# Performance work log

Measured on AMD Instinct MI355X. Metric: run time of the kernel, lower is better.

The kernel has to match this reference:

```python
import jax, jax.numpy as jnp
import numpy as np

N = 1_048_576   # flattened tokens
C = 128         # classes
IGNORE = 0
GAMMA = 1.0     # FocalLoss bug: alpha default (1) becomes self.gamma
BETA = 1.0      # ClassficationAndMDCA: self.beta = alpha = 1.0


def setup_inputs() -> dict:
    key = jax.random.key(0)
    k1, k2 = jax.random.split(key)
    inputs = jax.random.normal(k1, (N, C), dtype=jnp.float32)
    targets = jax.random.randint(k2, (N,), 0, C, dtype=jnp.int64)
    return {"inputs": inputs, "targets": targets}


def reference(inputs, targets):
    # ignore_index filtering expressed as masked reductions (jit-friendly)
    mask = (targets != IGNORE)
    maskf = mask.astype(inputs.dtype)               # [N]
    nvalid = jnp.sum(maskf)

    # Focal loss: -(1-pt)^gamma * log pt, mean over valid tokens
    logp = jax.nn.log_softmax(inputs, axis=1)       # [N, C]
    logpt = jnp.take_along_axis(logp, targets[:, None], axis=1)[:, 0]  # [N]
    pt = jnp.exp(logpt)
    focal = -((1.0 - pt) ** GAMMA) * logpt
    loss_cls = jnp.sum(focal * maskf) / nvalid

    # MDCA: per-class |mean confidence - mean label frequency|, mean over classes
    probs = jnp.exp(logp)                           # softmax, reuse log_softmax
    avg_conf = jnp.sum(probs * maskf[:, None], axis=0) / nvalid        # [C]
    avg_count = jnp.zeros((C,), inputs.dtype).at[targets].add(maskf) / nvalid  # [C]
    loss_cal = jnp.mean(jnp.abs(avg_conf - avg_count))

    return loss_cls + BETA * loss_cal
```

## Files before the change

kernel.cpp:

```cpp
#include <hip/hip_runtime.h>

#define NC 128
#define BLOCK 256
#define GRID 2048

__global__ void cmdca_init(float* __restrict__ acc) {
    int i = threadIdx.x;
    if (i < 2 * NC + 2) acc[i] = 0.0f;
}

__device__ __forceinline__ float half_sum32(float v) {
    v += __int_as_float(__builtin_amdgcn_ds_swizzle(__float_as_int(v), 0x041F));
    v += __int_as_float(__builtin_amdgcn_ds_swizzle(__float_as_int(v), 0x081F));
    v += __int_as_float(__builtin_amdgcn_ds_swizzle(__float_as_int(v), 0x101F));
    v += __int_as_float(__builtin_amdgcn_ds_swizzle(__float_as_int(v), 0x201F));
    v += __int_as_float(__builtin_amdgcn_ds_swizzle(__float_as_int(v), 0x401F));
    return v;
}

__global__ __launch_bounds__(BLOCK) void cmdca_main(const float* __restrict__ in,
                                                    const int* __restrict__ tgt,
                                                    float* __restrict__ acc,
                                                    int nrows) {
    const int lane  = threadIdx.x & 63;
    const int l31   = lane & 31;
    const int half  = lane >> 5;
    const int wave  = blockIdx.x * (BLOCK >> 6) + (threadIdx.x >> 6);
    const int nwaves = GRID * (BLOCK >> 6);

    float conf0 = 0.f, conf1 = 0.f, conf2 = 0.f, conf3 = 0.f;
    float cnt0  = 0.f, cnt1  = 0.f, cnt2  = 0.f, cnt3  = 0.f;
    float focal = 0.f, nval  = 0.f;

    auto process = [&](int pair) {
        int myrow = pair * 2 + half;
        int okrow = (myrow < nrows);
        int r = okrow ? myrow : (nrows - 1);
        const float4 x = *reinterpret_cast<const float4*>(in + (size_t)r * NC + l31 * 4);
        int t = tgt[r];
        float e0 = __expf(x.x), e1 = __expf(x.y), e2 = __expf(x.z), e3 = __expf(x.w);
        float s = half_sum32((e0 + e1) + (e2 + e3));
        float invs = 1.0f / s;
        float logZ = __logf(s);
        int te = t & 3;
        float xsel = (te == 0) ? x.x : (te == 1) ? x.y : (te == 2) ? x.z : x.w;
        int srclane = (lane & 32) + (t >> 2);
        float xt = __int_as_float(__builtin_amdgcn_ds_bpermute(srclane << 2,
                                                               __float_as_int(xsel)));
        float logpt = xt - logZ;
        float pt = __expf(logpt);
        float valid = (t != 0 && okrow) ? 1.0f : 0.0f;
        nval  += valid;
        focal += valid * (-(1.0f - pt) * logpt);
        float vs = valid * invs;
        conf0 += vs * e0; conf1 += vs * e1; conf2 += vs * e2; conf3 += vs * e3;
        float inc = (l31 == (t >> 2)) ? valid : 0.f;
        cnt0 += (te == 0) ? inc : 0.f;
        cnt1 += (te == 1) ? inc : 0.f;
        cnt2 += (te == 2) ? inc : 0.f;
        cnt3 += (te == 3) ? inc : 0.f;
    };

    const int npairs = (nrows + 1) >> 1;
    int p = wave;
    for (; p + nwaves < npairs; p += 2 * nwaves) {
        process(p);
        process(p + nwaves);
    }
    for (; p < npairs; p += nwaves) process(p);

    __shared__ float sconf[NC];
    __shared__ float scnt[NC];
    __shared__ float sfn[2];
    if (threadIdx.x < NC) { sconf[threadIdx.x] = 0.f; scnt[threadIdx.x] = 0.f; }
    if (threadIdx.x < 2)  sfn[threadIdx.x] = 0.f;
    __syncthreads();
    int cb = 4 * l31;
    atomicAdd(&sconf[cb + 0], conf0);
    atomicAdd(&sconf[cb + 1], conf1);
    atomicAdd(&sconf[cb + 2], conf2);
    atomicAdd(&sconf[cb + 3], conf3);
    atomicAdd(&scnt[cb + 0], cnt0);
    atomicAdd(&scnt[cb + 1], cnt1);
    atomicAdd(&scnt[cb + 2], cnt2);
    atomicAdd(&scnt[cb + 3], cnt3);
    if (l31 == 0) {
        atomicAdd(&sfn[0], focal);
        atomicAdd(&sfn[1], nval);
    }
    __syncthreads();
    if (threadIdx.x < NC) {
        atomicAdd(&acc[threadIdx.x],      sconf[threadIdx.x]);
        atomicAdd(&acc[NC + threadIdx.x], scnt[threadIdx.x]);
    }
    if (threadIdx.x == 0) {
        atomicAdd(&acc[2 * NC],     sfn[0]);
        atomicAdd(&acc[2 * NC + 1], sfn[1]);
    }
}

__global__ void cmdca_fin(const float* __restrict__ acc, float* __restrict__ out) {
    int c = threadIdx.x;
    float nvalid = acc[2 * NC + 1];
    float diff = fabsf(acc[c] - acc[NC + c]) / nvalid;
    #pragma unroll
    for (int o = 32; o; o >>= 1) diff += __shfl_xor(diff, o);
    __shared__ float sh[2];
    if ((threadIdx.x & 63) == 0) sh[threadIdx.x >> 6] = diff;
    __syncthreads();
    if (threadIdx.x == 0) {
        float loss_cal = (sh[0] + sh[1]) / (float)NC;
        float loss_cls = acc[2 * NC] / nvalid;
        out[0] = loss_cls + loss_cal;
    }
}

extern "C" void kernel_launch(void* const* d_in, const int* in_sizes, int n_in,
                              void* d_out, int out_size, void* d_ws, size_t ws_size,
                              hipStream_t stream) {
    const float* in  = (const float*)d_in[0];
    const int*   tgt = (const int*)d_in[1];
    float* out = (float*)d_out;
    float* acc = (float*)d_ws;
    int nrows = in_sizes[0] / NC;

    hipLaunchKernelGGL(cmdca_init, dim3(1), dim3(512), 0, stream, acc);
    hipLaunchKernelGGL(cmdca_main, dim3(GRID), dim3(BLOCK), 0, stream, in, tgt, acc, nrows);
    hipLaunchKernelGGL(cmdca_fin,  dim3(1), dim3(NC), 0, stream, acc, out);
}
```

Before: 146.6 us.

## Use DPP row reductions and readlane gathers, batch four row-pair loads before compute

Replaces the ds_swizzle half-wave sum with DPP row shifts/broadcast plus readlane of the half totals, and replaces the ds_bpermute target gather with scalar readlanes. The main loop now issues four independent row-pair loads before computing, so more memory requests are in flight per wave. Together these aim to cut LDS-path shuffle latency and expose more memory-level parallelism in a bandwidth-bound reduction, at the cost of higher register pressure from holding four float4s.

```diff
diff --git a/kernel.cpp b/kernel.cpp
--- a/kernel.cpp
+++ b/kernel.cpp
@@ -9,12 +9,18 @@
     if (i < 2 * NC + 2) acc[i] = 0.0f;
 }
 
-__device__ __forceinline__ float half_sum32(float v) {
-    v += __int_as_float(__builtin_amdgcn_ds_swizzle(__float_as_int(v), 0x041F));
-    v += __int_as_float(__builtin_amdgcn_ds_swizzle(__float_as_int(v), 0x081F));
-    v += __int_as_float(__builtin_amdgcn_ds_swizzle(__float_as_int(v), 0x101F));
-    v += __int_as_float(__builtin_amdgcn_ds_swizzle(__float_as_int(v), 0x201F));
-    v += __int_as_float(__builtin_amdgcn_ds_swizzle(__float_as_int(v), 0x401F));
+template <int CTRL>
+__device__ __forceinline__ float dpp_add(float v) {
+    int s = __builtin_amdgcn_update_dpp(0, __float_as_int(v), CTRL, 0xF, 0xF, true);
+    return v + __int_as_float(s);
+}
+
+__device__ __forceinline__ float half_sum_dpp(float v) {
+    v = dpp_add<0x111>(v);
+    v = dpp_add<0x112>(v);
+    v = dpp_add<0x114>(v);
+    v = dpp_add<0x118>(v);
+    v = dpp_add<0x142>(v);
     return v;
 }
 
@@ -32,24 +38,34 @@
     float cnt0  = 0.f, cnt1  = 0.f, cnt2  = 0.f, cnt3  = 0.f;
     float focal = 0.f, nval  = 0.f;
 
-    auto process = [&](int pair) {
+    auto load = [&](int pair, float4& x, int& t, int& ok) {
         int myrow = pair * 2 + half;
-        int okrow = (myrow < nrows);
-        int r = okrow ? myrow : (nrows - 1);
-        const float4 x = *reinterpret_cast<const float4*>(in + (size_t)r * NC + l31 * 4);
-        int t = tgt[r];
+        ok = (myrow < nrows);
+        int r = ok ? myrow : (nrows - 1);
+        x = *reinterpret_cast<const float4*>(in + (size_t)r * NC + l31 * 4);
+        t = tgt[r];
+    };
+
+    auto compute = [&](const float4& x, int t, int ok) {
         float e0 = __expf(x.x), e1 = __expf(x.y), e2 = __expf(x.z), e3 = __expf(x.w);
-        float s = half_sum32((e0 + e1) + (e2 + e3));
+        float sv = half_sum_dpp((e0 + e1) + (e2 + e3));
+        float s_lo = __int_as_float(__builtin_amdgcn_readlane(__float_as_int(sv), 31));
+        float s_hi = __int_as_float(__builtin_amdgcn_readlane(__float_as_int(sv), 63));
+        float s = half ? s_hi : s_lo;
         float invs = 1.0f / s;
         float logZ = __logf(s);
         int te = t & 3;
         float xsel = (te == 0) ? x.x : (te == 1) ? x.y : (te == 2) ? x.z : x.w;
-        int srclane = (lane & 32) + (t >> 2);
-        float xt = __int_as_float(__builtin_amdgcn_ds_bpermute(srclane << 2,
-                                                               __float_as_int(xsel)));
+        int t_lo = __builtin_amdgcn_readlane(t, 0);
+        int t_hi = __builtin_amdgcn_readlane(t, 32);
+        float xt_lo = __int_as_float(
+            __builtin_amdgcn_readlane(__float_as_int(xsel), t_lo >> 2));
+        float xt_hi = __int_as_float(
+            __builtin_amdgcn_readlane(__float_as_int(xsel), 32 + (t_hi >> 2)));
+        float xt = half ? xt_hi : xt_lo;
         float logpt = xt - logZ;
         float pt = __expf(logpt);
-        float valid = (t != 0 && okrow) ? 1.0f : 0.0f;
+        float valid = (t != 0 && ok) ? 1.0f : 0.0f;
         nval  += valid;
         focal += valid * (-(1.0f - pt) * logpt);
         float vs = valid * invs;
@@ -63,11 +79,22 @@
 
     const int npairs = (nrows + 1) >> 1;
     int p = wave;
-    for (; p + nwaves < npairs; p += 2 * nwaves) {
-        process(p);
-        process(p + nwaves);
+    for (; p + 3 * nwaves < npairs; p += 4 * nwaves) {
+        float4 x0, x1, x2, x3; int t0, t1, t2, t3, o0, o1, o2, o3;
+        load(p,              x0, t0, o0);
+        load(p + nwaves,     x1, t1, o1);
+        load(p + 2 * nwaves, x2, t2, o2);
+        load(p + 3 * nwaves, x3, t3, o3);
+        compute(x0, t0, o0);
+        compute(x1, t1, o1);
+        compute(x2, t2, o2);
+        compute(x3, t3, o3);
     }
-    for (; p < npairs; p += nwaves) process(p);
+    for (; p < npairs; p += nwaves) {
+        float4 x; int t, ok;
+        load(p, x, t, ok);
+        compute(x, t, ok);
+    }
 
     __shared__ float sconf[NC];
     __shared__ float scnt[NC];
```

New measurement: 135.3 us. 1.08x faster.
